# Kernel optimization log

Measured on AMD Instinct MI355X. Metric: run time of the kernel, lower is better.

The kernel has to match this reference:

```python
import jax, jax.numpy as jnp
import numpy as np

B, D_MODEL, N, H = 4, 256, 2048, 4
DIM = D_MODEL // H  # 64


def setup_inputs() -> dict:
    k = jax.random.key(0)
    ks = jax.random.split(k, 11)
    mk = lambda kk, shape, s=1.0: jax.random.normal(kk, shape, dtype=jnp.float32) * s
    return {
        'query': mk(ks[0], (B, D_MODEL, N)),
        'key': mk(ks[1], (B, D_MODEL, N)),
        'value': mk(ks[2], (B, D_MODEL, N)),
        # 1x1 Conv1d == per-position linear: weight [out, in], bias [out]
        'wq': mk(ks[3], (D_MODEL, D_MODEL), 0.05), 'bq': mk(ks[4], (D_MODEL,), 0.05),
        'wk': mk(ks[5], (D_MODEL, D_MODEL), 0.05), 'bk': mk(ks[6], (D_MODEL,), 0.05),
        'wv': mk(ks[7], (D_MODEL, D_MODEL), 0.05), 'bv': mk(ks[8], (D_MODEL,), 0.05),
        'wm': mk(ks[9], (D_MODEL, D_MODEL), 0.05), 'bm': mk(ks[10], (D_MODEL,), 0.05),
    }


def _proj(x, w, b):
    # Conv1d(kernel_size=1): [b, c_in, n] -> [b, c_out, n]
    return jnp.einsum('oc,bcn->bon', w, x) + b[None, :, None]


def reference(query, key, value, wq, bq, wk, bk, wv, bv, wm, bm):
    b = query.shape[0]
    # project and split channels d_model -> (dim, h); matches torch .view(b, dim, h, -1)
    q = _proj(query, wq, bq).reshape(b, DIM, H, -1)
    kk = _proj(key, wk, bk).reshape(b, DIM, H, -1)
    v = _proj(value, wv, bv).reshape(b, DIM, H, -1)
    scores = jnp.einsum('bdhn,bdhm->bhnm', q, kk) / jnp.sqrt(jnp.float32(DIM))
    prob = jax.nn.softmax(scores, axis=-1)  # [b, h, n, m]
    x = jnp.einsum('bhnm,bdhm->bdhn', prob, v)
    return _proj(x.reshape(b, DIM * H, -1), wm, bm)
```

## Files before the change

### kernel.cpp

```cpp
#include <hip/hip_runtime.h>

#define DMODEL 256
#define NSEQ   2048
#define NB     4
#define NH     4
#define DHEAD  64

typedef __attribute__((ext_vector_type(8))) short short8;
typedef __attribute__((ext_vector_type(4))) float float4v;
typedef __attribute__((ext_vector_type(2))) unsigned int uint2v;
typedef unsigned short u16;

static __device__ inline u16 f2bf(float f) {
    unsigned u = __builtin_bit_cast(unsigned, f);
    u += 0x7fffu + ((u >> 16) & 1u);
    return (u16)(u >> 16);
}
static __device__ inline unsigned pack2bf(float a, float b) {
    return (unsigned)f2bf(a) | ((unsigned)f2bf(b) << 16);
}

__global__ __launch_bounds__(256) void proj_qkv_kernel(
    const float* __restrict__ xq, const float* __restrict__ xk, const float* __restrict__ xv,
    const float* __restrict__ wqp, const float* __restrict__ wkp, const float* __restrict__ wvp,
    const float* __restrict__ bqp, const float* __restrict__ bkp, const float* __restrict__ bvp,
    u16* __restrict__ q_ws, u16* __restrict__ k_ws, u16* __restrict__ vt_ws)
{
    const int nt0 = blockIdx.x;
    const int ot  = blockIdx.y;
    const int bz  = blockIdx.z;
    const int b = bz / 3, mode = bz % 3;

    const float* X  = (mode == 0) ? xq : (mode == 1) ? xk : xv;
    const float* W  = (mode == 0) ? wqp : (mode == 1) ? wkp : wvp;
    const float* BI = (mode == 0) ? bqp : (mode == 1) ? bkp : bvp;
    X += (size_t)b * DMODEL * NSEQ;

    const int tid = threadIdx.x;
    const int wave = tid >> 6, lane = tid & 63;
    const int g = lane >> 4, ql = lane & 15;

    __shared__ u16 xt[64][72];
    __shared__ u16 wt[64][72];

    float4v acc[4];
    #pragma unroll
    for (int i = 0; i < 4; i++) acc[i] = (float4v){0.f, 0.f, 0.f, 0.f};

    const int obase = ot * 64, nbase = nt0 * 64;

    for (int c0 = 0; c0 < DMODEL; c0 += 64) {
        #pragma unroll
        for (int i = 0; i < 4; i++) {
            int e = tid + i * 256;
            int c = e >> 4, n4 = (e & 15) * 4;
            float4v xv4 = *(const float4v*)&X[(size_t)(c0 + c) * NSEQ + nbase + n4];
            xt[n4 + 0][c] = f2bf(xv4[0]);
            xt[n4 + 1][c] = f2bf(xv4[1]);
            xt[n4 + 2][c] = f2bf(xv4[2]);
            xt[n4 + 3][c] = f2bf(xv4[3]);
        }
        #pragma unroll
        for (int i = 0; i < 4; i++) {
            int e = tid + i * 256;
            int orow = e >> 4, c4 = (e & 15) * 4;
            int og = (orow & 48) | ((orow & 3) << 2) | ((orow >> 2) & 3);
            float4v wv4 = *(const float4v*)&W[(size_t)(obase + og) * DMODEL + c0 + c4];
            unsigned* dst = (unsigned*)&wt[orow][c4];
            dst[0] = pack2bf(wv4[0], wv4[1]);
            dst[1] = pack2bf(wv4[2], wv4[3]);
        }
        __syncthreads();
        #pragma unroll
        for (int kc = 0; kc < 2; kc++) {
            short8 afrag = *(const short8*)&wt[wave * 16 + ql][kc * 32 + g * 8];
            #pragma unroll
            for (int nt = 0; nt < 4; nt++) {
                short8 bfrag = *(const short8*)&xt[nt * 16 + ql][kc * 32 + g * 8];
                acc[nt] = __builtin_amdgcn_mfma_f32_16x16x32_bf16(afrag, bfrag, acc[nt], 0, 0, 0);
            }
        }
        __syncthreads();
    }

    const int h = g;
    const int d0 = (obase + wave * 16) >> 2;
    float bias[4];
    #pragma unroll
    for (int r = 0; r < 4; r++) bias[r] = BI[obase + wave * 16 + 4 * r + g];

    #pragma unroll
    for (int nt = 0; nt < 4; nt++) {
        int n = nbase + nt * 16 + ql;
        float v[4];
        #pragma unroll
        for (int r = 0; r < 4; r++) v[r] = acc[nt][r] + bias[r];
        if (mode == 0) {
            #pragma unroll
            for (int r = 0; r < 4; r++) v[r] *= 0.18033688011112042f;
            uint2v pk = {pack2bf(v[0], v[1]), pack2bf(v[2], v[3])};
            *(uint2v*)&q_ws[((size_t)(b * NH + h) * NSEQ + n) * DHEAD + d0] = pk;
        } else if (mode == 1) {
            uint2v pk = {pack2bf(v[0], v[1]), pack2bf(v[2], v[3])};
            *(uint2v*)&k_ws[((size_t)(b * NH + h) * NSEQ + n) * DHEAD + d0] = pk;
        } else {
            #pragma unroll
            for (int r = 0; r < 4; r++)
                vt_ws[((size_t)(b * NH + h) * DHEAD + d0 + r) * NSEQ + n] = f2bf(v[r]);
        }
    }
}

__global__ __launch_bounds__(256) void attn_kernel(
    const u16* __restrict__ q_ws, const u16* __restrict__ k_ws,
    const u16* __restrict__ vt_ws, u16* __restrict__ x_ws)
{
    const int bid = blockIdx.x;
    const int orig = (bid & 7) * 32 + (bid >> 3);
    const int bh = orig >> 4;
    const int qt128 = orig & 15;
    const int b = bh >> 2, h = bh & 3;

    const int tid = threadIdx.x;
    const int wave = tid >> 6, lane = tid & 63;
    const int g = lane >> 4, ql = lane & 15;
    const int qbase = qt128 * 128 + wave * 32;

    const u16* qp = q_ws + ((size_t)bh * NSEQ + qbase) * DHEAD;
    const u16* kp = k_ws + (size_t)bh * NSEQ * DHEAD;
    const u16* vp = vt_ws + (size_t)bh * DHEAD * NSEQ;

    __shared__ u16 kt[2][64][64];
    __shared__ u16 vt[2][64][64];
    __shared__ u16 p_lds[4][2][16][72];

    const int srow = lane >> 3;
    const int su_l = lane & 7;
    const int u_l  = su_l ^ srow;
    const int swz  = ql & 7;

    short8 qf[2][2];
    #pragma unroll
    for (int qt = 0; qt < 2; qt++)
        #pragma unroll
        for (int kc = 0; kc < 2; kc++)
            qf[qt][kc] = *(const short8*)(qp + (size_t)(qt * 16 + ql) * DHEAD + kc * 32 + g * 8);

    float4v acc[2][4];
    #pragma unroll
    for (int qt = 0; qt < 2; qt++)
        #pragma unroll
        for (int t = 0; t < 4; t++) acc[qt][t] = (float4v){0.f, 0.f, 0.f, 0.f};
    float m0 = -INFINITY, m1 = -INFINITY, l0 = 0.f, l1 = 0.f;

    #define STAGE(mb_, bufi_)                                                          \
        {                                                                              \
            _Pragma("unroll")                                                          \
            for (int i_ = 0; i_ < 2; i_++) {                                           \
                int row_ = wave * 16 + i_ * 8 + srow;                                  \
                __builtin_amdgcn_global_load_lds(                                      \
                    (const __attribute__((address_space(1))) unsigned int*)            \
                        (kp + (size_t)((mb_) + row_) * DHEAD + u_l * 8),               \
                    (__attribute__((address_space(3))) unsigned int*)                  \
                        &kt[bufi_][wave * 16 + i_ * 8][0],                             \
                    16, 0, 0);                                                         \
                __builtin_amdgcn_global_load_lds(                                      \
                    (const __attribute__((address_space(1))) unsigned int*)            \
                        (vp + (size_t)row_ * NSEQ + (mb_) + u_l * 8),                  \
                    (__attribute__((address_space(3))) unsigned int*)                  \
                        &vt[bufi_][wave * 16 + i_ * 8][0],                             \
                    16, 0, 0);                                                         \
            }                                                                          \
        }

    STAGE(0, 0);
    __syncthreads();

    int buf = 0;
    for (int t = 0; t < NSEQ / 64; t++) {
        const int mb = t * 64;
        if (t < NSEQ / 64 - 1) STAGE(mb + 64, buf ^ 1);

        float4v st[2][4];
        #pragma unroll
        for (int qt = 0; qt < 2; qt++)
            #pragma unroll
            for (int mt = 0; mt < 4; mt++) st[qt][mt] = (float4v){0.f, 0.f, 0.f, 0.f};
        #pragma unroll
        for (int mt = 0; mt < 4; mt++) {
            #pragma unroll
            for (int kc = 0; kc < 2; kc++) {
                short8 kf = *(const short8*)&kt[buf][mt * 16 + ql][((kc * 4 + g) ^ swz) * 8];
                st[0][mt] = __builtin_amdgcn_mfma_f32_16x16x32_bf16(kf, qf[0][kc], st[0][mt], 0, 0, 0);
                st[1][mt] = __builtin_amdgcn_mfma_f32_16x16x32_bf16(kf, qf[1][kc], st[1][mt], 0, 0, 0);
            }
        }

        float tmax0 = -INFINITY, tmax1 = -INFINITY;
        #pragma unroll
        for (int mt = 0; mt < 4; mt++)
            #pragma unroll
            for (int r = 0; r < 4; r++) {
                tmax0 = fmaxf(tmax0, st[0][mt][r]);
                tmax1 = fmaxf(tmax1, st[1][mt][r]);
            }
        tmax0 = fmaxf(tmax0, __shfl_xor(tmax0, 16, 64));
        tmax0 = fmaxf(tmax0, __shfl_xor(tmax0, 32, 64));
        tmax1 = fmaxf(tmax1, __shfl_xor(tmax1, 16, 64));
        tmax1 = fmaxf(tmax1, __shfl_xor(tmax1, 32, 64));

        bool need = (tmax0 > m0 + 8.f) || (tmax1 > m1 + 8.f);
        if (__any(need)) {
            float mn0 = fmaxf(m0, tmax0), mn1 = fmaxf(m1, tmax1);
            float a0 = __builtin_amdgcn_exp2f(m0 - mn0);
            float a1 = __builtin_amdgcn_exp2f(m1 - mn1);
            #pragma unroll
            for (int tt = 0; tt < 4; tt++)
                #pragma unroll
                for (int r = 0; r < 4; r++) {
                    acc[0][tt][r] *= a0;
                    acc[1][tt][r] *= a1;
                }
            l0 *= a0; l1 *= a1;
            m0 = mn0; m1 = mn1;
        }

        float ps0 = 0.f, ps1 = 0.f;
        #pragma unroll
        for (int mt = 0; mt < 4; mt++) {
            float p0[4], p1[4];
            #pragma unroll
            for (int r = 0; r < 4; r++) {
                p0[r] = __builtin_amdgcn_exp2f(st[0][mt][r] - m0);
                p1[r] = __builtin_amdgcn_exp2f(st[1][mt][r] - m1);
                ps0 += p0[r];
                ps1 += p1[r];
            }
            unsigned* d0p = (unsigned*)&p_lds[wave][0][ql][mt * 16 + g * 4];
            d0p[0] = pack2bf(p0[0], p0[1]);
            d0p[1] = pack2bf(p0[2], p0[3]);
            unsigned* d1p = (unsigned*)&p_lds[wave][1][ql][mt * 16 + g * 4];
            d1p[0] = pack2bf(p1[0], p1[1]);
            d1p[1] = pack2bf(p1[2], p1[3]);
        }
        ps0 += __shfl_xor(ps0, 16, 64);
        ps0 += __shfl_xor(ps0, 32, 64);
        ps1 += __shfl_xor(ps1, 16, 64);
        ps1 += __shfl_xor(ps1, 32, 64);
        l0 += ps0; l1 += ps1;

        #pragma unroll
        for (int kc = 0; kc < 2; kc++) {
            short8 pf0 = *(const short8*)&p_lds[wave][0][ql][kc * 32 + g * 8];
            short8 pf1 = *(const short8*)&p_lds[wave][1][ql][kc * 32 + g * 8];
            #pragma unroll
            for (int tt = 0; tt < 4; tt++) {
                short8 vf = *(const short8*)&vt[buf][tt * 16 + ql][((kc * 4 + g) ^ swz) * 8];
                acc[0][tt] = __builtin_amdgcn_mfma_f32_16x16x32_bf16(vf, pf0, acc[0][tt], 0, 0, 0);
                acc[1][tt] = __builtin_amdgcn_mfma_f32_16x16x32_bf16(vf, pf1, acc[1][tt], 0, 0, 0);
            }
        }
        __syncthreads();
        buf ^= 1;
    }
    #undef STAGE

    float inv0 = 1.f / l0, inv1 = 1.f / l1;
    #pragma unroll
    for (int qt = 0; qt < 2; qt++) {
        float inv = qt ? inv1 : inv0;
        #pragma unroll
        for (int t = 0; t < 4; t++)
            #pragma unroll
            for (int r = 0; r < 4; r++) {
                int d = t * 16 + g * 4 + r;
                int c = d * NH + h;
                x_ws[((size_t)b * DMODEL + c) * NSEQ + qbase + qt * 16 + ql] = f2bf(acc[qt][t][r] * inv);
            }
    }
}

__global__ __launch_bounds__(256) void proj_out_kernel(
    const u16* __restrict__ xw, const float* __restrict__ wm,
    const float* __restrict__ bm, float* __restrict__ out)
{
    const int nt0 = blockIdx.x, ot = blockIdx.y, b = blockIdx.z;
    const u16* X = xw + (size_t)b * DMODEL * NSEQ;

    const int tid = threadIdx.x;
    const int wave = tid >> 6, lane = tid & 63;
    const int g = lane >> 4, ql = lane & 15;

    __shared__ u16 xt[64][72];
    __shared__ u16 wt[64][72];

    float4v acc[4];
    #pragma unroll
    for (int i = 0; i < 4; i++) acc[i] = (float4v){0.f, 0.f, 0.f, 0.f};

    const int obase = ot * 64, nbase = nt0 * 64;

    for (int c0 = 0; c0 < DMODEL; c0 += 64) {
        #pragma unroll
        for (int i = 0; i < 2; i++) {
            int e = tid + i * 256;
            int c = e >> 3, n8 = (e & 7) * 8;
            short8 xv8 = *(const short8*)&X[(size_t)(c0 + c) * NSEQ + nbase + n8];
            #pragma unroll
            for (int j = 0; j < 8; j++) xt[n8 + j][c] = (u16)xv8[j];
        }
        #pragma unroll
        for (int i = 0; i < 4; i++) {
            int e = tid + i * 256;
            int orow = e >> 4, c4 = (e & 15) * 4;
            float4v wv4 = *(const float4v*)&wm[(size_t)(obase + orow) * DMODEL + c0 + c4];
            unsigned* dst = (unsigned*)&wt[orow][c4];
            dst[0] = pack2bf(wv4[0], wv4[1]);
            dst[1] = pack2bf(wv4[2], wv4[3]);
        }
        __syncthreads();
        #pragma unroll
        for (int kc = 0; kc < 2; kc++) {
            short8 afrag = *(const short8*)&wt[wave * 16 + ql][kc * 32 + g * 8];
            #pragma unroll
            for (int nt = 0; nt < 4; nt++) {
                short8 bfrag = *(const short8*)&xt[nt * 16 + ql][kc * 32 + g * 8];
                acc[nt] = __builtin_amdgcn_mfma_f32_16x16x32_bf16(afrag, bfrag, acc[nt], 0, 0, 0);
            }
        }
        __syncthreads();
    }

    const int o0 = obase + wave * 16 + g * 4;
    #pragma unroll
    for (int nt = 0; nt < 4; nt++) {
        int n = nbase + nt * 16 + ql;
        #pragma unroll
        for (int r = 0; r < 4; r++) {
            int o = o0 + r;
            out[((size_t)b * DMODEL + o) * NSEQ + n] = acc[nt][r] + bm[o];
        }
    }
}

extern "C" void kernel_launch(void* const* d_in, const int* in_sizes, int n_in,
                              void* d_out, int out_size, void* d_ws, size_t ws_size,
                              hipStream_t stream)
{
    const float* query = (const float*)d_in[0];
    const float* key   = (const float*)d_in[1];
    const float* value = (const float*)d_in[2];
    const float* wq = (const float*)d_in[3];
    const float* bq = (const float*)d_in[4];
    const float* wk = (const float*)d_in[5];
    const float* bk = (const float*)d_in[6];
    const float* wv = (const float*)d_in[7];
    const float* bv = (const float*)d_in[8];
    const float* wm = (const float*)d_in[9];
    const float* bm = (const float*)d_in[10];
    float* out = (float*)d_out;

    char* ws = (char*)d_ws;
    const size_t SEG = (size_t)NB * NH * NSEQ * DHEAD * sizeof(u16);
    u16* q_ws  = (u16*)(ws);
    u16* k_ws  = (u16*)(ws + SEG);
    u16* vt_ws = (u16*)(ws + 2 * SEG);
    u16* x_ws  = (u16*)(ws + 3 * SEG);

    proj_qkv_kernel<<<dim3(32, 4, 12), 256, 0, stream>>>(
        query, key, value, wq, wk, wv, bq, bk, bv, q_ws, k_ws, vt_ws);
    attn_kernel<<<dim3(256), 256, 0, stream>>>(q_ws, k_ws, vt_ws, x_ws);
    proj_out_kernel<<<dim3(32, 4, NB), 256, 0, stream>>>(x_ws, wm, bm, out);
}
```

Baseline: 171.1 us.

## Pre-convert inputs and weights to bf16 and use async LDS loads in projections

Adds a separate kernel that converts and transposes the fp32 inputs to bf16 in [n, c] layout, and a kernel that packs all four weight matrices to bf16 with the head permutation already applied. The projection GEMMs then stream tiles with double-buffered global_load_lds into swizzled LDS instead of doing per-element conversion and transposed scalar LDS stores. Attention now writes its output in a head-major row layout with vectorized stores so the output projection can load it directly. The softmax max and sum are also restructured slightly. This trades two extra kernel launches and an extra round trip of the bf16 input copy through memory for cheaper, overlapped GEMM loads.

```diff
diff --git a/kernel.cpp b/kernel.cpp
--- a/kernel.cpp
+++ b/kernel.cpp
@@ -1,4 +1,5 @@
 #include <hip/hip_runtime.h>
+#include <hip/hip_bf16.h>
 
 #define DMODEL 256
 #define NSEQ   2048
@@ -8,80 +9,154 @@
 
 typedef __attribute__((ext_vector_type(8))) short short8;
 typedef __attribute__((ext_vector_type(4))) float float4v;
+typedef __attribute__((ext_vector_type(2))) float float2v;
 typedef __attribute__((ext_vector_type(2))) unsigned int uint2v;
 typedef unsigned short u16;
+
+#define AS1 __attribute__((address_space(1)))
+#define AS3 __attribute__((address_space(3)))
 
 static __device__ inline u16 f2bf(float f) {
     unsigned u = __builtin_bit_cast(unsigned, f);
     u += 0x7fffu + ((u >> 16) & 1u);
     return (u16)(u >> 16);
 }
-static __device__ inline unsigned pack2bf(float a, float b) {
-    return (unsigned)f2bf(a) | ((unsigned)f2bf(b) << 16);
+static __device__ inline unsigned pk2(float a, float b) {
+    __hip_bfloat162 h = __float22bfloat162_rn(make_float2(a, b));
+    unsigned r;
+    __builtin_memcpy(&r, &h, 4);
+    return r;
+}
+static __device__ inline float max3f(float a, float b, float c) {
+    return fmaxf(fmaxf(a, b), c);
+}
+static __device__ inline float tmax16(const float4v* s) {
+    float a = max3f(s[0][0], s[0][1], s[0][2]);
+    float b = max3f(s[0][3], s[1][0], s[1][1]);
+    float c = max3f(s[1][2], s[1][3], s[2][0]);
+    float d = max3f(s[2][1], s[2][2], s[2][3]);
+    float e = max3f(s[3][0], s[3][1], s[3][2]);
+    float f = max3f(a, b, c);
+    float g = max3f(d, e, s[3][3]);
+    return fmaxf(f, g);
+}
+
+__global__ __launch_bounds__(256) void convert_x_kernel(
+    const float* __restrict__ xq, const float* __restrict__ xk,
+    const float* __restrict__ xv, u16* __restrict__ xt_ws)
+{
+    const int nt = blockIdx.x;
+    const int ct = blockIdx.y;
+    const int z  = blockIdx.z;
+    const int b = z / 3, mode = z % 3;
+    const float* X = ((mode == 0) ? xq : (mode == 1) ? xk : xv) + (size_t)b * DMODEL * NSEQ;
+    u16* dst = xt_ws + (size_t)z * NSEQ * DMODEL;
+
+    __shared__ u16 t[64][72];
+    const int tid = threadIdx.x;
+
+    #pragma unroll
+    for (int i = 0; i < 4; i++) {
+        int e = tid + i * 256;
+        int c = e >> 4;
+        int n4 = (e & 15) * 4;
+        float4v v = *(const float4v*)&X[(size_t)(ct * 64 + c) * NSEQ + nt * 64 + n4];
+        #pragma unroll
+        for (int j = 0; j < 4; j++) {
+            int row = n4 + j;
+            int fr = (row & 7) ^ ((row >> 3) & 7);
+            t[row][(((c >> 3) ^ fr) << 3) + (c & 7)] = f2bf(v[j]);
+        }
+    }
+    __syncthreads();
+    #pragma unroll
+    for (int i = 0; i < 4; i++) {
+        int e = tid + i * 256;
+        int n = e >> 4;
+        int cb = (e & 15) * 4;
+        int fr = (n & 7) ^ ((n >> 3) & 7);
+        uint2v val = *(const uint2v*)&t[n][(((cb >> 3) ^ fr) << 3) + (cb & 7)];
+        *(uint2v*)&dst[(size_t)(nt * 64 + n) * DMODEL + ct * 64 + cb] = val;
+    }
+}
+
+__global__ __launch_bounds__(256) void wpack_kernel(
+    const float* __restrict__ wq, const float* __restrict__ wk,
+    const float* __restrict__ wv, const float* __restrict__ wm,
+    u16* __restrict__ wbf)
+{
+    const int sr = blockIdx.x, m = blockIdx.y, tcol = threadIdx.x;
+    const float* W = (m == 0) ? wq : (m == 1) ? wk : (m == 2) ? wv : wm;
+    float v;
+    if (m < 3) {
+        int og = (sr & ~15) | ((sr & 3) << 2) | ((sr >> 2) & 3);
+        v = W[(size_t)og * DMODEL + tcol];
+    } else {
+        int c = ((tcol & 63) << 2) | (tcol >> 6);
+        v = W[(size_t)sr * DMODEL + c];
+    }
+    wbf[(size_t)m * 65536 + (size_t)sr * DMODEL + tcol] = f2bf(v);
 }
 
 __global__ __launch_bounds__(256) void proj_qkv_kernel(
-    const float* __restrict__ xq, const float* __restrict__ xk, const float* __restrict__ xv,
-    const float* __restrict__ wqp, const float* __restrict__ wkp, const float* __restrict__ wvp,
+    const u16* __restrict__ xt_ws, const u16* __restrict__ wbf,
     const float* __restrict__ bqp, const float* __restrict__ bkp, const float* __restrict__ bvp,
     u16* __restrict__ q_ws, u16* __restrict__ k_ws, u16* __restrict__ vt_ws)
 {
-    const int nt0 = blockIdx.x;
-    const int ot  = blockIdx.y;
-    const int bz  = blockIdx.z;
+    const int nt0 = blockIdx.x, ot = blockIdx.y, bz = blockIdx.z;
     const int b = bz / 3, mode = bz % 3;
-
-    const float* X  = (mode == 0) ? xq : (mode == 1) ? xk : xv;
-    const float* W  = (mode == 0) ? wqp : (mode == 1) ? wkp : wvp;
     const float* BI = (mode == 0) ? bqp : (mode == 1) ? bkp : bvp;
-    X += (size_t)b * DMODEL * NSEQ;
 
     const int tid = threadIdx.x;
     const int wave = tid >> 6, lane = tid & 63;
     const int g = lane >> 4, ql = lane & 15;
-
-    __shared__ u16 xt[64][72];
-    __shared__ u16 wt[64][72];
+    const int srow8 = lane >> 3, su = lane & 7;
+    const int u_l = su ^ srow8;
+    const int obase = ot * 64, nbase = nt0 * 64;
+
+    const u16* Asrc = wbf + (size_t)mode * 65536;
+    const u16* Bsrc = xt_ws + (size_t)bz * (NSEQ * DMODEL);
+
+    __shared__ u16 at[2][64][64];
+    __shared__ u16 bt[2][64][64];
 
     float4v acc[4];
     #pragma unroll
     for (int i = 0; i < 4; i++) acc[i] = (float4v){0.f, 0.f, 0.f, 0.f};
 
-    const int obase = ot * 64, nbase = nt0 * 64;
-
-    for (int c0 = 0; c0 < DMODEL; c0 += 64) {
-        #pragma unroll
-        for (int i = 0; i < 4; i++) {
-            int e = tid + i * 256;
-            int c = e >> 4, n4 = (e & 15) * 4;
-            float4v xv4 = *(const float4v*)&X[(size_t)(c0 + c) * NSEQ + nbase + n4];
-            xt[n4 + 0][c] = f2bf(xv4[0]);
-            xt[n4 + 1][c] = f2bf(xv4[1]);
-            xt[n4 + 2][c] = f2bf(xv4[2]);
-            xt[n4 + 3][c] = f2bf(xv4[3]);
-        }
-        #pragma unroll
-        for (int i = 0; i < 4; i++) {
-            int e = tid + i * 256;
-            int orow = e >> 4, c4 = (e & 15) * 4;
-            int og = (orow & 48) | ((orow & 3) << 2) | ((orow >> 2) & 3);
-            float4v wv4 = *(const float4v*)&W[(size_t)(obase + og) * DMODEL + c0 + c4];
-            unsigned* dst = (unsigned*)&wt[orow][c4];
-            dst[0] = pack2bf(wv4[0], wv4[1]);
-            dst[1] = pack2bf(wv4[2], wv4[3]);
-        }
-        __syncthreads();
+    #define PSTAGE(bufi_, c0_)                                                         \
+        { _Pragma("unroll")                                                            \
+          for (int p_ = 0; p_ < 2; p_++) {                                             \
+            int rb_ = wave * 8 + p_ * 32;                                              \
+            int row_ = rb_ + srow8;                                                    \
+            __builtin_amdgcn_global_load_lds(                                          \
+                (const AS1 unsigned int*)(Asrc + (size_t)(obase + row_) * DMODEL + (c0_) + u_l * 8), \
+                (AS3 unsigned int*)&at[bufi_][rb_][0], 16, 0, 0);                      \
+            __builtin_amdgcn_global_load_lds(                                          \
+                (const AS1 unsigned int*)(Bsrc + (size_t)(nbase + row_) * DMODEL + (c0_) + u_l * 8), \
+                (AS3 unsigned int*)&bt[bufi_][rb_][0], 16, 0, 0);                      \
+          } }
+
+    PSTAGE(0, 0)
+    __syncthreads();
+    int buf = 0;
+    const int sw = ql & 7;
+    #pragma unroll
+    for (int t = 0; t < 4; t++) {
+        if (t < 3) PSTAGE(buf ^ 1, (t + 1) * 64)
         #pragma unroll
         for (int kc = 0; kc < 2; kc++) {
-            short8 afrag = *(const short8*)&wt[wave * 16 + ql][kc * 32 + g * 8];
+            short8 afrag = *(const short8*)&at[buf][wave * 16 + ql][(((kc * 4 + g) ^ sw)) * 8];
             #pragma unroll
             for (int nt = 0; nt < 4; nt++) {
-                short8 bfrag = *(const short8*)&xt[nt * 16 + ql][kc * 32 + g * 8];
+                short8 bfrag = *(const short8*)&bt[buf][nt * 16 + ql][(((kc * 4 + g) ^ sw)) * 8];
                 acc[nt] = __builtin_amdgcn_mfma_f32_16x16x32_bf16(afrag, bfrag, acc[nt], 0, 0, 0);
             }
         }
         __syncthreads();
-    }
+        buf ^= 1;
+    }
+    #undef PSTAGE
 
     const int h = g;
     const int d0 = (obase + wave * 16) >> 2;
@@ -98,10 +173,10 @@
         if (mode == 0) {
             #pragma unroll
             for (int r = 0; r < 4; r++) v[r] *= 0.18033688011112042f;
-            uint2v pk = {pack2bf(v[0], v[1]), pack2bf(v[2], v[3])};
+            uint2v pk = {pk2(v[0], v[1]), pk2(v[2], v[3])};
             *(uint2v*)&q_ws[((size_t)(b * NH + h) * NSEQ + n) * DHEAD + d0] = pk;
         } else if (mode == 1) {
-            uint2v pk = {pack2bf(v[0], v[1]), pack2bf(v[2], v[3])};
+            uint2v pk = {pk2(v[0], v[1]), pk2(v[2], v[3])};
             *(uint2v*)&k_ws[((size_t)(b * NH + h) * NSEQ + n) * DHEAD + d0] = pk;
         } else {
             #pragma unroll
@@ -113,14 +188,12 @@
 
 __global__ __launch_bounds__(256) void attn_kernel(
     const u16* __restrict__ q_ws, const u16* __restrict__ k_ws,
-    const u16* __restrict__ vt_ws, u16* __restrict__ x_ws)
+    const u16* __restrict__ vt_ws, u16* __restrict__ x_hs)
 {
     const int bid = blockIdx.x;
     const int orig = (bid & 7) * 32 + (bid >> 3);
     const int bh = orig >> 4;
     const int qt128 = orig & 15;
-    const int b = bh >> 2, h = bh & 3;
-
     const int tid = threadIdx.x;
     const int wave = tid >> 6, lane = tid & 63;
     const int g = lane >> 4, ql = lane & 15;
@@ -159,17 +232,11 @@
             for (int i_ = 0; i_ < 2; i_++) {                                           \
                 int row_ = wave * 16 + i_ * 8 + srow;                                  \
                 __builtin_amdgcn_global_load_lds(                                      \
-                    (const __attribute__((address_space(1))) unsigned int*)            \
-                        (kp + (size_t)((mb_) + row_) * DHEAD + u_l * 8),               \
-                    (__attribute__((address_space(3))) unsigned int*)                  \
-                        &kt[bufi_][wave * 16 + i_ * 8][0],                             \
-                    16, 0, 0);                                                         \
+                    (const AS1 unsigned int*)(kp + (size_t)((mb_) + row_) * DHEAD + u_l * 8), \
+                    (AS3 unsigned int*)&kt[bufi_][wave * 16 + i_ * 8][0], 16, 0, 0);   \
                 __builtin_amdgcn_global_load_lds(                                      \
-                    (const __attribute__((address_space(1))) unsigned int*)            \
-                        (vp + (size_t)row_ * NSEQ + (mb_) + u_l * 8),                  \
-                    (__attribute__((address_space(3))) unsigned int*)                  \
-                        &vt[bufi_][wave * 16 + i_ * 8][0],                             \
-                    16, 0, 0);                                                         \
+                    (const AS1 unsigned int*)(vp + (size_t)row_ * NSEQ + (mb_) + u_l * 8), \
+                    (AS3 unsigned int*)&vt[bufi_][wave * 16 + i_ * 8][0], 16, 0, 0);   \
             }                                                                          \
         }
 
@@ -196,14 +263,8 @@
             }
         }
 
-        float tmax0 = -INFINITY, tmax1 = -INFINITY;
-        #pragma unroll
-        for (int mt = 0; mt < 4; mt++)
-            #pragma unroll
-            for (int r = 0; r < 4; r++) {
-                tmax0 = fmaxf(tmax0, st[0][mt][r]);
-                tmax1 = fmaxf(tmax1, st[1][mt][r]);
-            }
+        float tmax0 = tmax16(&st[0][0]);
+        float tmax1 = tmax16(&st[1][0]);
         tmax0 = fmaxf(tmax0, __shfl_xor(tmax0, 16, 64));
         tmax0 = fmaxf(tmax0, __shfl_xor(tmax0, 32, 64));
         tmax1 = fmaxf(tmax1, __shfl_xor(tmax1, 16, 64));
@@ -225,24 +286,25 @@
             m0 = mn0; m1 = mn1;
         }
 
-        float ps0 = 0.f, ps1 = 0.f;
+        float2v s0v = {0.f, 0.f}, s1v = {0.f, 0.f};
         #pragma unroll
         for (int mt = 0; mt < 4; mt++) {
-            float p0[4], p1[4];
-            #pragma unroll
-            for (int r = 0; r < 4; r++) {
-                p0[r] = __builtin_amdgcn_exp2f(st[0][mt][r] - m0);
-                p1[r] = __builtin_amdgcn_exp2f(st[1][mt][r] - m1);
-                ps0 += p0[r];
-                ps1 += p1[r];
-            }
-            unsigned* d0p = (unsigned*)&p_lds[wave][0][ql][mt * 16 + g * 4];
-            d0p[0] = pack2bf(p0[0], p0[1]);
-            d0p[1] = pack2bf(p0[2], p0[3]);
-            unsigned* d1p = (unsigned*)&p_lds[wave][1][ql][mt * 16 + g * 4];
-            d1p[0] = pack2bf(p1[0], p1[1]);
-            d1p[1] = pack2bf(p1[2], p1[3]);
-        }
+            float p00 = __builtin_amdgcn_exp2f(st[0][mt][0] - m0);
+            float p01 = __builtin_amdgcn_exp2f(st[0][mt][1] - m0);
+            float p02 = __builtin_amdgcn_exp2f(st[0][mt][2] - m0);
+            float p03 = __builtin_amdgcn_exp2f(st[0][mt][3] - m0);
+            s0v += (float2v){p00, p01};
+            s0v += (float2v){p02, p03};
+            *(uint2v*)&p_lds[wave][0][ql][mt * 16 + g * 4] = (uint2v){pk2(p00, p01), pk2(p02, p03)};
+            float p10 = __builtin_amdgcn_exp2f(st[1][mt][0] - m1);
+            float p11 = __builtin_amdgcn_exp2f(st[1][mt][1] - m1);
+            float p12 = __builtin_amdgcn_exp2f(st[1][mt][2] - m1);
+            float p13 = __builtin_amdgcn_exp2f(st[1][mt][3] - m1);
+            s1v += (float2v){p10, p11};
+            s1v += (float2v){p12, p13};
+            *(uint2v*)&p_lds[wave][1][ql][mt * 16 + g * 4] = (uint2v){pk2(p10, p11), pk2(p12, p13)};
+        }
+        float ps0 = s0v[0] + s0v[1], ps1 = s1v[0] + s1v[1];
         ps0 += __shfl_xor(ps0, 16, 64);
         ps0 += __shfl_xor(ps0, 32, 64);
         ps1 += __shfl_xor(ps1, 16, 64);
@@ -269,67 +331,71 @@
     #pragma unroll
     for (int qt = 0; qt < 2; qt++) {
         float inv = qt ? inv1 : inv0;
-        #pragma unroll
-        for (int t = 0; t < 4; t++)
-            #pragma unroll
-            for (int r = 0; r < 4; r++) {
-                int d = t * 16 + g * 4 + r;
-                int c = d * NH + h;
-                x_ws[((size_t)b * DMODEL + c) * NSEQ + qbase + qt * 16 + ql] = f2bf(acc[qt][t][r] * inv);
-            }
+        u16* xrow = x_hs + ((size_t)bh * NSEQ + qbase + qt * 16 + ql) * DHEAD;
+        #pragma unroll
+        for (int t = 0; t < 4; t++) {
+            uint2v pk = {pk2(acc[qt][t][0] * inv, acc[qt][t][1] * inv),
+                         pk2(acc[qt][t][2] * inv, acc[qt][t][3] * inv)};
+            *(uint2v*)&xrow[t * 16 + g * 4] = pk;
+        }
     }
 }
 
 __global__ __launch_bounds__(256) void proj_out_kernel(
-    const u16* __restrict__ xw, const float* __restrict__ wm,
+    const u16* __restrict__ x_hs, const u16* __restrict__ wbf,
     const float* __restrict__ bm, float* __restrict__ out)
 {
     const int nt0 = blockIdx.x, ot = blockIdx.y, b = blockIdx.z;
-    const u16* X = xw + (size_t)b * DMODEL * NSEQ;
 
     const int tid = threadIdx.x;
     const int wave = tid >> 6, lane = tid & 63;
     const int g = lane >> 4, ql = lane & 15;
-
-    __shared__ u16 xt[64][72];
-    __shared__ u16 wt[64][72];
+    const int srow8 = lane >> 3, su = lane & 7;
+    const int u_l = su ^ srow8;
+    const int obase = ot * 64, nbase = nt0 * 64;
+
+    const u16* Asrc = wbf + (size_t)3 * 65536;
+
+    __shared__ u16 at[2][64][64];
+    __shared__ u16 bt[2][64][64];
 
     float4v acc[4];
     #pragma unroll
     for (int i = 0; i < 4; i++) acc[i] = (float4v){0.f, 0.f, 0.f, 0.f};
 
-    const int obase = ot * 64, nbase = nt0 * 64;
-
-    for (int c0 = 0; c0 < DMODEL; c0 += 64) {
-        #pragma unroll
-        for (int i = 0; i < 2; i++) {
-            int e = tid + i * 256;
-            int c = e >> 3, n8 = (e & 7) * 8;
-            short8 xv8 = *(const short8*)&X[(size_t)(c0 + c) * NSEQ + nbase + n8];
-            #pragma unroll
-            for (int j = 0; j < 8; j++) xt[n8 + j][c] = (u16)xv8[j];
-        }
-        #pragma unroll
-        for (int i = 0; i < 4; i++) {
-            int e = tid + i * 256;
-            int orow = e >> 4, c4 = (e & 15) * 4;
-            float4v wv4 = *(const float4v*)&wm[(size_t)(obase + orow) * DMODEL + c0 + c4];
-            unsigned* dst = (unsigned*)&wt[orow][c4];
-            dst[0] = pack2bf(wv4[0], wv4[1]);
-            dst[1] = pack2bf(wv4[2], wv4[3]);
-        }
-        __syncthreads();
+    #define OSTAGE(bufi_, c0_)                                                         \
+        { _Pragma("unroll")                                                            \
+          for (int p_ = 0; p_ < 2; p_++) {                                             \
+            int rb_ = wave * 8 + p_ * 32;                                              \
+            int row_ = rb_ + srow8;                                                    \
+            __builtin_amdgcn_global_load_lds(                                          \
+                (const AS1 unsigned int*)(Asrc + (size_t)(obase + row_) * DMODEL + (c0_) + u_l * 8), \
+                (AS3 unsigned int*)&at[bufi_][rb_][0], 16, 0, 0);                      \
+            __builtin_amdgcn_global_load_lds(                                          \
+                (const AS1 unsigned int*)(x_hs + ((size_t)(b * NH + ((c0_) >> 6)) * NSEQ + nbase + row_) * DHEAD + u_l * 8), \
+                (AS3 unsigned int*)&bt[bufi_][rb_][0], 16, 0, 0);                      \
+          } }
+
+    OSTAGE(0, 0)
+    __syncthreads();
+    int buf = 0;
+    const int sw = ql & 7;
+    #pragma unroll
+    for (int t = 0; t < 4; t++) {
+        if (t < 3) OSTAGE(buf ^ 1, (t + 1) * 64)
         #pragma unroll
         for (int kc = 0; kc < 2; kc++) {
-            short8 afrag = *(const short8*)&wt[wave * 16 + ql][kc * 32 + g * 8];
+            short8 afrag = *(const short8*)&at[buf][wave * 16 + ql][(((kc * 4 + g) ^ sw)) * 8];
             #pragma unroll
             for (int nt = 0; nt < 4; nt++) {
-                short8 bfrag = *(const short8*)&xt[nt * 16 + ql][kc * 32 + g * 8];
+                short8 bfrag = *(const short8*)&bt[buf][nt * 16 + ql][(((kc * 4 + g) ^ sw)) * 8];
                 acc[nt] = __builtin_amdgcn_mfma_f32_16x16x32_bf16(afrag, bfrag, acc[nt], 0, 0, 0);
             }
         }
         __syncthreads();
-    }
+        buf ^= 1;
+    }
+    #undef OSTAGE
 
     const int o0 = obase + wave * 16 + g * 4;
     #pragma unroll
@@ -365,10 +431,14 @@
     u16* q_ws  = (u16*)(ws);
     u16* k_ws  = (u16*)(ws + SEG);
     u16* vt_ws = (u16*)(ws + 2 * SEG);
-    u16* x_ws  = (u16*)(ws + 3 * SEG);
-
+    u16* x_hs  = (u16*)(ws + 3 * SEG);
+    u16* xt_ws = (u16*)(ws + 4 * SEG);
+    u16* wbf   = (u16*)(ws + 4 * SEG + (size_t)12 * NSEQ * DMODEL * sizeof(u16));
+
+    convert_x_kernel<<<dim3(32, 4, 12), 256, 0, stream>>>(query, key, value, xt_ws);
+    wpack_kernel<<<dim3(256, 4), 256, 0, stream>>>(wq, wk, wv, wm, wbf);
     proj_qkv_kernel<<<dim3(32, 4, 12), 256, 0, stream>>>(
-        query, key, value, wq, wk, wv, bq, bk, bv, q_ws, k_ws, vt_ws);
-    attn_kernel<<<dim3(256), 256, 0, stream>>>(q_ws, k_ws, vt_ws, x_ws);
-    proj_out_kernel<<<dim3(32, 4, NB), 256, 0, stream>>>(x_ws, wm, bm, out);
-}
+        xt_ws, wbf, bq, bk, bv, q_ws, k_ws, vt_ws);
+    attn_kernel<<<dim3(256), 256, 0, stream>>>(q_ws, k_ws, vt_ws, x_hs);
+    proj_out_kernel<<<dim3(32, 4, NB), 256, 0, stream>>>(x_hs, wbf, bm, out);
+}
```

Measured after the change: 162.5 us. 1.05x faster.
